# Performance work log

Measured on AMD Instinct MI355X. Metric: run time of the kernel, lower is better.

Reference implementation:

```python
import jax, jax.numpy as jnp
import numpy as np

N = 50000          # nodes
E = 500000         # edges (before self-loops)
IN_C = 128
OUT_C = 32
HEADS = 8
NEG_SLOPE = 0.2    # PyG GATConv default


def setup_inputs() -> dict:
    key = jax.random.key(0)
    k1, k2, k3, k4, k5 = jax.random.split(key, 5)
    x = jax.random.normal(k1, (N, IN_C), dtype=jnp.float32)
    edge_index = jax.random.randint(k2, (2, E), 0, N, dtype=jnp.int32)
    # learned params (PyG GATConv: shared lin, att_src/att_dst vectors, bias)
    s = 1.0 / np.sqrt(IN_C)
    W = jax.random.normal(k3, (IN_C, HEADS * OUT_C), dtype=jnp.float32) * s
    att_src = jax.random.normal(k4, (1, HEADS, OUT_C), dtype=jnp.float32) * s
    att_dst = jax.random.normal(k5, (1, HEADS, OUT_C), dtype=jnp.float32) * s
    bias = jnp.zeros((HEADS * OUT_C,), dtype=jnp.float32)
    return {"x": x, "edge_index": edge_index, "W": W,
            "att_src": att_src, "att_dst": att_dst, "bias": bias}


def reference(x, edge_index, W, att_src, att_dst, bias):
    n = x.shape[0]
    H, C = att_src.shape[1], att_src.shape[2]
    # Linear projection -> [N, H, C]
    xw = (x @ W).reshape(n, H, C)
    # Per-node attention logits [N, H]
    a_src = jnp.sum(xw * att_src, axis=-1)
    a_dst = jnp.sum(xw * att_dst, axis=-1)
    # add self-loops (PyG default add_self_loops=True)
    loop = jnp.arange(n, dtype=edge_index.dtype)
    src = jnp.concatenate([edge_index[0], loop])
    dst = jnp.concatenate([edge_index[1], loop])
    # edge scores: LeakyReLU(alpha_src[j] + alpha_dst[i])  -> [E+N, H]
    alpha = jax.nn.leaky_relu(a_src[src] + a_dst[dst], NEG_SLOPE)
    # segment softmax over edges grouped by destination node
    amax = jax.lax.stop_gradient(jax.ops.segment_max(alpha, dst, num_segments=n))
    alpha = jnp.exp(alpha - amax[dst])
    denom = jax.ops.segment_sum(alpha, dst, num_segments=n)
    alpha = alpha / (denom[dst] + 1e-16)
    # weighted messages and scatter-add aggregation
    msg = xw[src] * alpha[:, :, None]          # [E+N, H, C]
    out = jax.ops.segment_sum(msg, dst, num_segments=n)  # [N, H, C]
    return out.reshape(n, H * C) + bias
```

## Files before the change

### kernel.cpp

```cpp
#include <hip/hip_runtime.h>
#include <stdint.h>

#define N_NODES 50000
#define HC 256
#define IN_C 128
#define CAP 64
#define GEMM_BLKS 3125
#define EPB 160

typedef __bf16 v8bf __attribute__((ext_vector_type(8)));
typedef float  v4f  __attribute__((ext_vector_type(4)));

__device__ __forceinline__ uint16_t f2bf(float f) {
    union { float f; uint32_t i; } c; c.f = f;
    uint32_t x = c.i;
    uint32_t r = x + 0x7fffu + ((x >> 16) & 1u);
    return (uint16_t)(r >> 16);
}
__device__ __forceinline__ uint16_t f2h(float f) {
    union { _Float16 h; uint16_t u; } c;
    c.h = (_Float16)f;
    return c.u;
}
__device__ __forceinline__ void h8(uint4 u, float* f) {
    union { uint32_t i; _Float16 h[2]; } c;
    c.i = u.x; f[0] = (float)c.h[0]; f[1] = (float)c.h[1];
    c.i = u.y; f[2] = (float)c.h[0]; f[3] = (float)c.h[1];
    c.i = u.z; f[4] = (float)c.h[0]; f[5] = (float)c.h[1];
    c.i = u.w; f[6] = (float)c.h[0]; f[7] = (float)c.h[1];
}
__device__ __forceinline__ void ld4h(uint2 u, float& f0, float& f1, float& f2, float& f3) {
    union { uint32_t i; _Float16 h[2]; } c;
    c.i = u.x; f0 = (float)c.h[0]; f1 = (float)c.h[1];
    c.i = u.y; f2 = (float)c.h[0]; f3 = (float)c.h[1];
}
__device__ __forceinline__ float hexp2(float x) {
    return __builtin_amdgcn_exp2f(x);
}

__global__ void k_wt(const float* __restrict__ W, uint16_t* __restrict__ Wt,
                     int* __restrict__ cnt) {
    int idx = blockIdx.x * 256 + threadIdx.x;
    int k = idx >> 8;
    int c = idx & 255;
    Wt[c * IN_C + k] = f2bf(W[idx]);
    if (idx < 25000) *(int2*)(cnt + idx * 2) = make_int2(0, 0);
}

__global__ __launch_bounds__(256) void k_gemm_fill(const float* __restrict__ x,
                                                   const uint16_t* __restrict__ Wt,
                                                   const float* __restrict__ att_src,
                                                   const float* __restrict__ att_dst,
                                                   uint16_t* __restrict__ xwh,
                                                   float* __restrict__ a_src,
                                                   float* __restrict__ a_dst,
                                                   const int* __restrict__ src,
                                                   const int* __restrict__ dst,
                                                   int* __restrict__ cnt,
                                                   int* __restrict__ slots,
                                                   int E) {
    __shared__ uint16_t lsm[16 * 272];
    uint16_t* lx = lsm;
    uint16_t* lc = lsm;
    int t  = threadIdx.x;
    int nb = blockIdx.x * 16;

    int e = blockIdx.x * EPB + t;
    bool has = (t < EPB) && (e < E);
    int ed = 0, es = 0;
    if (has) { ed = dst[e]; es = src[e]; }

    {
        int row = t >> 4, c8 = (t & 15) * 8;
        const float4* p = (const float4*)(x + (size_t)(nb + row) * IN_C + c8);
        float4 p0 = p[0], p1 = p[1];
        v8bf a;
        a[0] = (__bf16)p0.x; a[1] = (__bf16)p0.y; a[2] = (__bf16)p0.z; a[3] = (__bf16)p0.w;
        a[4] = (__bf16)p1.x; a[5] = (__bf16)p1.y; a[6] = (__bf16)p1.z; a[7] = (__bf16)p1.w;
        *(v8bf*)(lx + row * 136 + c8) = a;
    }
    __syncthreads();

    int w = t >> 6, lane = t & 63;
    int m = lane & 15, g = lane >> 4;
    v4f acc[4];
#pragma unroll
    for (int ct = 0; ct < 4; ++ct) acc[ct] = (v4f){0.f, 0.f, 0.f, 0.f};
    const uint16_t* lxp = lx + m * 136 + g * 8;
    const uint16_t* wp  = Wt + (size_t)(w * 64 + m) * IN_C + g * 8;
#pragma unroll
    for (int s = 0; s < 4; ++s) {
        v8bf a = *(const v8bf*)(lxp + s * 32);
#pragma unroll
        for (int ct = 0; ct < 4; ++ct) {
            v8bf b = *(const v8bf*)(wp + (size_t)ct * 16 * IN_C + s * 32);
            acc[ct] = __builtin_amdgcn_mfma_f32_16x16x32_bf16(a, b, acc[ct], 0, 0, 0);
        }
    }
    __syncthreads();

#pragma unroll
    for (int ct = 0; ct < 4; ++ct) {
        int cols = w * 64 + ((ct ^ g) << 4) + m;
#pragma unroll
        for (int r = 0; r < 4; ++r) {
            lc[(g * 4 + r) * 272 + cols] = f2h(acc[ct][r]);
        }
    }
    __syncthreads();

    {
        int row = t >> 4;
        int c   = t & 15;
        int gg  = row >> 2;
        int sc0 = c ^ (gg << 1);
        int sc1 = sc0 + 16;
        const uint16_t* lr = lc + row * 272;
        uint4 u0 = *(const uint4*)(lr + sc0 * 8);
        uint4 u1 = *(const uint4*)(lr + sc1 * 8);
        size_t gb = (size_t)(nb + row) * HC + c * 8;
        *(uint4*)(xwh + gb)       = u0;
        *(uint4*)(xwh + gb + 128) = u1;

        float f0[8], f1[8];
        h8(u0, f0);
        h8(u1, f1);
        float4 as0 = *(const float4*)(att_src + c * 8);
        float4 as1 = *(const float4*)(att_src + c * 8 + 4);
        float4 as2 = *(const float4*)(att_src + 128 + c * 8);
        float4 as3 = *(const float4*)(att_src + 128 + c * 8 + 4);
        float4 ad0 = *(const float4*)(att_dst + c * 8);
        float4 ad1 = *(const float4*)(att_dst + c * 8 + 4);
        float4 ad2 = *(const float4*)(att_dst + 128 + c * 8);
        float4 ad3 = *(const float4*)(att_dst + 128 + c * 8 + 4);

        float ps0 = f0[0]*as0.x + f0[1]*as0.y + f0[2]*as0.z + f0[3]*as0.w
                  + f0[4]*as1.x + f0[5]*as1.y + f0[6]*as1.z + f0[7]*as1.w;
        float pd0 = f0[0]*ad0.x + f0[1]*ad0.y + f0[2]*ad0.z + f0[3]*ad0.w
                  + f0[4]*ad1.x + f0[5]*ad1.y + f0[6]*ad1.z + f0[7]*ad1.w;
        float ps1 = f1[0]*as2.x + f1[1]*as2.y + f1[2]*as2.z + f1[3]*as2.w
                  + f1[4]*as3.x + f1[5]*as3.y + f1[6]*as3.z + f1[7]*as3.w;
        float pd1 = f1[0]*ad2.x + f1[1]*ad2.y + f1[2]*ad2.z + f1[3]*ad2.w
                  + f1[4]*ad3.x + f1[5]*ad3.y + f1[6]*ad3.z + f1[7]*ad3.w;

        ps0 += __shfl_xor(ps0, 1, 64); ps0 += __shfl_xor(ps0, 2, 64);
        ps1 += __shfl_xor(ps1, 1, 64); ps1 += __shfl_xor(ps1, 2, 64);
        pd0 += __shfl_xor(pd0, 1, 64); pd0 += __shfl_xor(pd0, 2, 64);
        pd1 += __shfl_xor(pd1, 1, 64); pd1 += __shfl_xor(pd1, 2, 64);
        if ((c & 3) == 0) {
            const float LOG2E = 1.44269504f;
            int node = nb + row;
            int h = c >> 2;
            a_src[node * 8 + h]     = ps0 * LOG2E;
            a_src[node * 8 + 4 + h] = ps1 * LOG2E;
            a_dst[node * 8 + h]     = pd0 * LOG2E;
            a_dst[node * 8 + 4 + h] = pd1 * LOG2E;
        }
    }

    if (has) {
        int pos = atomicAdd(&cnt[ed], 1);
        slots[(size_t)ed * CAP + pos] = es;
    }
}

__global__ __launch_bounds__(256) void k_agg(const uint16_t* __restrict__ xwh,
                                             const float* __restrict__ a_src,
                                             const float* __restrict__ a_dst,
                                             const int* __restrict__ cnt,
                                             const int* __restrict__ slots,
                                             const float* __restrict__ bias,
                                             float* __restrict__ out) {
    int i    = blockIdx.x * 4 + (threadIdx.x >> 6);
    int lane = threadIdx.x & 63;
    int h = lane >> 3;
    float sdst = a_dst[i * 8 + h];

    float s0 = a_src[i * 8 + h] + sdst;
    s0 = fmaxf(s0, 0.2f * s0);
    float p0 = hexp2(s0);
    float l = p0;
    uint2 us = *(const uint2*)(xwh + (size_t)i * HC + lane * 4);
    float sx0, sx1, sx2, sx3;
    ld4h(us, sx0, sx1, sx2, sx3);
    float a0 = p0 * sx0, a1 = p0 * sx1, a2 = p0 * sx2, a3 = p0 * sx3;

    int n     = cnt[i];
    int start = i * CAP;
    int end   = start + n;
    int e = start;
    for (; e + 8 <= end; e += 8) {
        uint2 uu[8];
        float sa[8];
#pragma unroll
        for (int k = 0; k < 8; ++k) {
            int j = __builtin_amdgcn_readfirstlane(slots[e + k]);
            uu[k] = *(const uint2*)(xwh + (size_t)j * HC + lane * 4);
            sa[k] = a_src[j * 8 + h];
        }
#pragma unroll
        for (int k = 0; k < 8; ++k) {
            float s = sa[k] + sdst;
            s = fmaxf(s, 0.2f * s);
            float w = hexp2(s);
            l += w;
            float g0, g1, g2, g3;
            ld4h(uu[k], g0, g1, g2, g3);
            a0 = fmaf(w, g0, a0); a1 = fmaf(w, g1, a1);
            a2 = fmaf(w, g2, a2); a3 = fmaf(w, g3, a3);
        }
    }
    if (e < end) {
        uint2 uu[8];
        float sa[8];
#pragma unroll
        for (int k = 0; k < 8; ++k) {
            int jr = __builtin_amdgcn_readfirstlane(slots[e + k]);
            uint32_t j = min((uint32_t)jr, (uint32_t)(N_NODES - 1));
            uu[k] = *(const uint2*)(xwh + (size_t)j * HC + lane * 4);
            sa[k] = a_src[j * 8 + h];
        }
#pragma unroll
        for (int k = 0; k < 8; ++k) {
            float s = sa[k] + sdst;
            s = fmaxf(s, 0.2f * s);
            float w = (e + k < end) ? hexp2(s) : 0.f;
            l += w;
            float g0, g1, g2, g3;
            ld4h(uu[k], g0, g1, g2, g3);
            a0 = fmaf(w, g0, a0); a1 = fmaf(w, g1, a1);
            a2 = fmaf(w, g2, a2); a3 = fmaf(w, g3, a3);
        }
    }

    float inv = 1.f / (l + 1e-16f);
    float4 b = *(const float4*)(bias + lane * 4);
    float4 o;
    o.x = fmaf(a0, inv, b.x);
    o.y = fmaf(a1, inv, b.y);
    o.z = fmaf(a2, inv, b.z);
    o.w = fmaf(a3, inv, b.w);
    *(float4*)(out + (size_t)i * HC + lane * 4) = o;
}

extern "C" void kernel_launch(void* const* d_in, const int* in_sizes, int n_in,
                              void* d_out, int out_size, void* d_ws, size_t ws_size,
                              hipStream_t stream) {
    const float* x       = (const float*)d_in[0];
    const int*   ei      = (const int*)d_in[1];
    const float* W       = (const float*)d_in[2];
    const float* att_src = (const float*)d_in[3];
    const float* att_dst = (const float*)d_in[4];
    const float* bias    = (const float*)d_in[5];
    float*       out     = (float*)d_out;

    const int E = in_sizes[1] / 2;
    const int* src = ei;
    const int* dst = ei + E;

    char* ws = (char*)d_ws;
    uint16_t* xwh   = (uint16_t*)(ws);
    uint16_t* Wt    = (uint16_t*)(ws + 25600000);
    float*    a_src = (float*)   (ws + 25665536);
    float*    a_dst = (float*)   (ws + 27265536);
    int*      cnt   = (int*)     (ws + 28865536);
    int*      slots = (int*)     (ws + 29065536);

    k_wt<<<128, 256, 0, stream>>>(W, Wt, cnt);
    k_gemm_fill<<<GEMM_BLKS, 256, 0, stream>>>(x, Wt, att_src, att_dst,
                                               xwh, a_src, a_dst,
                                               src, dst, cnt, slots, E);
    k_agg<<<12500, 256, 0, stream>>>(xwh, a_src, a_dst, cnt, slots, bias, out);
}
```

Baseline: 174.5 us.

## Process 64 nodes per GEMM block to reuse W fragments across subtiles

Each GEMM block now handles 64 nodes instead of 16. W B-fragments are loaded once per k-step and reused across four 16-row subtiles, so blocks drop from 3125 to 782 and W traffic shrinks. Each block takes 640 edges (up to three per thread), and the edge-slot atomics now run right after staging x so they overlap the MFMA work. The cost is more registers (16 accumulators), launch_bounds(256,4), a serialized per-subtile epilogue with extra barriers, and bounds checks for the partial last block.

Result: no change. 174.7 us (+0.1%).

```diff
diff --git a/kernel.cpp b/kernel.cpp
--- a/kernel.cpp
+++ b/kernel.cpp
@@ -5,8 +5,9 @@
 #define HC 256
 #define IN_C 128
 #define CAP 64
-#define GEMM_BLKS 3125
-#define EPB 160
+#define NPB 64
+#define GEMM_BLKS 782
+#define EPB 640
 
 typedef __bf16 v8bf __attribute__((ext_vector_type(8)));
 typedef float  v4f  __attribute__((ext_vector_type(4)));
@@ -47,120 +48,148 @@
     if (idx < 25000) *(int2*)(cnt + idx * 2) = make_int2(0, 0);
 }
 
-__global__ __launch_bounds__(256) void k_gemm_fill(const float* __restrict__ x,
-                                                   const uint16_t* __restrict__ Wt,
-                                                   const float* __restrict__ att_src,
-                                                   const float* __restrict__ att_dst,
-                                                   uint16_t* __restrict__ xwh,
-                                                   float* __restrict__ a_src,
-                                                   float* __restrict__ a_dst,
-                                                   const int* __restrict__ src,
-                                                   const int* __restrict__ dst,
-                                                   int* __restrict__ cnt,
-                                                   int* __restrict__ slots,
-                                                   int E) {
-    __shared__ uint16_t lsm[16 * 272];
+__global__ __launch_bounds__(256, 4) void k_gemm_fill(const float* __restrict__ x,
+                                                      const uint16_t* __restrict__ Wt,
+                                                      const float* __restrict__ att_src,
+                                                      const float* __restrict__ att_dst,
+                                                      uint16_t* __restrict__ xwh,
+                                                      float* __restrict__ a_src,
+                                                      float* __restrict__ a_dst,
+                                                      const int* __restrict__ src,
+                                                      const int* __restrict__ dst,
+                                                      int* __restrict__ cnt,
+                                                      int* __restrict__ slots,
+                                                      int E) {
+    __shared__ uint16_t lsm[64 * 136];
     uint16_t* lx = lsm;
     uint16_t* lc = lsm;
     int t  = threadIdx.x;
-    int nb = blockIdx.x * 16;
-
-    int e = blockIdx.x * EPB + t;
-    bool has = (t < EPB) && (e < E);
-    int ed = 0, es = 0;
-    if (has) { ed = dst[e]; es = src[e]; }
+    int nb = blockIdx.x * NPB;
+
+    int e0 = blockIdx.x * EPB + t;
+    int e1 = e0 + 256;
+    int e2 = e0 + 512;
+    bool h0 = (e0 < E);
+    bool h1 = (e1 < E);
+    bool h2 = (t < 128) && (e2 < E);
+    int d0 = 0, s0 = 0, d1 = 0, s1 = 0, d2 = 0, s2 = 0;
+    if (h0) { d0 = dst[e0]; s0 = src[e0]; }
+    if (h1) { d1 = dst[e1]; s1 = src[e1]; }
+    if (h2) { d2 = dst[e2]; s2 = src[e2]; }
 
     {
-        int row = t >> 4, c8 = (t & 15) * 8;
-        const float4* p = (const float4*)(x + (size_t)(nb + row) * IN_C + c8);
-        float4 p0 = p[0], p1 = p[1];
-        v8bf a;
-        a[0] = (__bf16)p0.x; a[1] = (__bf16)p0.y; a[2] = (__bf16)p0.z; a[3] = (__bf16)p0.w;
-        a[4] = (__bf16)p1.x; a[5] = (__bf16)p1.y; a[6] = (__bf16)p1.z; a[7] = (__bf16)p1.w;
-        *(v8bf*)(lx + row * 136 + c8) = a;
+        int rr = t >> 4, c8 = (t & 15) * 8;
+#pragma unroll
+        for (int u = 0; u < 4; ++u) {
+            int row = rr + u * 16;
+            int nr  = nb + row;
+            v8bf a;
+#pragma unroll
+            for (int q = 0; q < 8; ++q) a[q] = (__bf16)0.f;
+            if (nr < N_NODES) {
+                const float4* p = (const float4*)(x + (size_t)nr * IN_C + c8);
+                float4 p0 = p[0], p1 = p[1];
+                a[0] = (__bf16)p0.x; a[1] = (__bf16)p0.y; a[2] = (__bf16)p0.z; a[3] = (__bf16)p0.w;
+                a[4] = (__bf16)p1.x; a[5] = (__bf16)p1.y; a[6] = (__bf16)p1.z; a[7] = (__bf16)p1.w;
+            }
+            *(v8bf*)(lx + row * 136 + c8) = a;
+        }
     }
     __syncthreads();
+
+    if (h0) { int pos = atomicAdd(&cnt[d0], 1); slots[(size_t)d0 * CAP + pos] = s0; }
+    if (h1) { int pos = atomicAdd(&cnt[d1], 1); slots[(size_t)d1 * CAP + pos] = s1; }
+    if (h2) { int pos = atomicAdd(&cnt[d2], 1); slots[(size_t)d2 * CAP + pos] = s2; }
 
     int w = t >> 6, lane = t & 63;
     int m = lane & 15, g = lane >> 4;
-    v4f acc[4];
-#pragma unroll
-    for (int ct = 0; ct < 4; ++ct) acc[ct] = (v4f){0.f, 0.f, 0.f, 0.f};
-    const uint16_t* lxp = lx + m * 136 + g * 8;
-    const uint16_t* wp  = Wt + (size_t)(w * 64 + m) * IN_C + g * 8;
+    v4f acc[4][4];
+#pragma unroll
+    for (int st = 0; st < 4; ++st)
+#pragma unroll
+        for (int ct = 0; ct < 4; ++ct) acc[st][ct] = (v4f){0.f, 0.f, 0.f, 0.f};
+
+    const uint16_t* wp = Wt + (size_t)(w * 64 + m) * IN_C + g * 8;
 #pragma unroll
     for (int s = 0; s < 4; ++s) {
-        v8bf a = *(const v8bf*)(lxp + s * 32);
+        v8bf b0 = *(const v8bf*)(wp + (size_t)0 * 16 * IN_C + s * 32);
+        v8bf b1 = *(const v8bf*)(wp + (size_t)1 * 16 * IN_C + s * 32);
+        v8bf b2 = *(const v8bf*)(wp + (size_t)2 * 16 * IN_C + s * 32);
+        v8bf b3 = *(const v8bf*)(wp + (size_t)3 * 16 * IN_C + s * 32);
+#pragma unroll
+        for (int st = 0; st < 4; ++st) {
+            v8bf a = *(const v8bf*)(lx + (st * 16 + m) * 136 + g * 8 + s * 32);
+            acc[st][0] = __builtin_amdgcn_mfma_f32_16x16x32_bf16(a, b0, acc[st][0], 0, 0, 0);
+            acc[st][1] = __builtin_amdgcn_mfma_f32_16x16x32_bf16(a, b1, acc[st][1], 0, 0, 0);
+            acc[st][2] = __builtin_amdgcn_mfma_f32_16x16x32_bf16(a, b2, acc[st][2], 0, 0, 0);
+            acc[st][3] = __builtin_amdgcn_mfma_f32_16x16x32_bf16(a, b3, acc[st][3], 0, 0, 0);
+        }
+    }
+    __syncthreads();
+
+#pragma unroll
+    for (int st = 0; st < 4; ++st) {
 #pragma unroll
         for (int ct = 0; ct < 4; ++ct) {
-            v8bf b = *(const v8bf*)(wp + (size_t)ct * 16 * IN_C + s * 32);
-            acc[ct] = __builtin_amdgcn_mfma_f32_16x16x32_bf16(a, b, acc[ct], 0, 0, 0);
-        }
-    }
-    __syncthreads();
-
-#pragma unroll
-    for (int ct = 0; ct < 4; ++ct) {
-        int cols = w * 64 + ((ct ^ g) << 4) + m;
-#pragma unroll
-        for (int r = 0; r < 4; ++r) {
-            lc[(g * 4 + r) * 272 + cols] = f2h(acc[ct][r]);
-        }
-    }
-    __syncthreads();
-
-    {
-        int row = t >> 4;
-        int c   = t & 15;
-        int gg  = row >> 2;
-        int sc0 = c ^ (gg << 1);
-        int sc1 = sc0 + 16;
-        const uint16_t* lr = lc + row * 272;
-        uint4 u0 = *(const uint4*)(lr + sc0 * 8);
-        uint4 u1 = *(const uint4*)(lr + sc1 * 8);
-        size_t gb = (size_t)(nb + row) * HC + c * 8;
-        *(uint4*)(xwh + gb)       = u0;
-        *(uint4*)(xwh + gb + 128) = u1;
-
-        float f0[8], f1[8];
-        h8(u0, f0);
-        h8(u1, f1);
-        float4 as0 = *(const float4*)(att_src + c * 8);
-        float4 as1 = *(const float4*)(att_src + c * 8 + 4);
-        float4 as2 = *(const float4*)(att_src + 128 + c * 8);
-        float4 as3 = *(const float4*)(att_src + 128 + c * 8 + 4);
-        float4 ad0 = *(const float4*)(att_dst + c * 8);
-        float4 ad1 = *(const float4*)(att_dst + c * 8 + 4);
-        float4 ad2 = *(const float4*)(att_dst + 128 + c * 8);
-        float4 ad3 = *(const float4*)(att_dst + 128 + c * 8 + 4);
-
-        float ps0 = f0[0]*as0.x + f0[1]*as0.y + f0[2]*as0.z + f0[3]*as0.w
-                  + f0[4]*as1.x + f0[5]*as1.y + f0[6]*as1.z + f0[7]*as1.w;
-        float pd0 = f0[0]*ad0.x + f0[1]*ad0.y + f0[2]*ad0.z + f0[3]*ad0.w
-                  + f0[4]*ad1.x + f0[5]*ad1.y + f0[6]*ad1.z + f0[7]*ad1.w;
-        float ps1 = f1[0]*as2.x + f1[1]*as2.y + f1[2]*as2.z + f1[3]*as2.w
-                  + f1[4]*as3.x + f1[5]*as3.y + f1[6]*as3.z + f1[7]*as3.w;
-        float pd1 = f1[0]*ad2.x + f1[1]*ad2.y + f1[2]*ad2.z + f1[3]*ad2.w
-                  + f1[4]*ad3.x + f1[5]*ad3.y + f1[6]*ad3.z + f1[7]*ad3.w;
-
-        ps0 += __shfl_xor(ps0, 1, 64); ps0 += __shfl_xor(ps0, 2, 64);
-        ps1 += __shfl_xor(ps1, 1, 64); ps1 += __shfl_xor(ps1, 2, 64);
-        pd0 += __shfl_xor(pd0, 1, 64); pd0 += __shfl_xor(pd0, 2, 64);
-        pd1 += __shfl_xor(pd1, 1, 64); pd1 += __shfl_xor(pd1, 2, 64);
-        if ((c & 3) == 0) {
-            const float LOG2E = 1.44269504f;
-            int node = nb + row;
-            int h = c >> 2;
-            a_src[node * 8 + h]     = ps0 * LOG2E;
-            a_src[node * 8 + 4 + h] = ps1 * LOG2E;
-            a_dst[node * 8 + h]     = pd0 * LOG2E;
-            a_dst[node * 8 + 4 + h] = pd1 * LOG2E;
-        }
-    }
-
-    if (has) {
-        int pos = atomicAdd(&cnt[ed], 1);
-        slots[(size_t)ed * CAP + pos] = es;
+            int cols = w * 64 + ((ct ^ g) << 4) + m;
+#pragma unroll
+            for (int r = 0; r < 4; ++r) {
+                lc[(g * 4 + r) * 272 + cols] = f2h(acc[st][ct][r]);
+            }
+        }
+        __syncthreads();
+
+        {
+            int row = t >> 4;
+            int c   = t & 15;
+            int gg  = row >> 2;
+            int sc0 = c ^ (gg << 1);
+            int sc1 = sc0 + 16;
+            const uint16_t* lr = lc + row * 272;
+            uint4 u0 = *(const uint4*)(lr + sc0 * 8);
+            uint4 u1 = *(const uint4*)(lr + sc1 * 8);
+            int node = nb + st * 16 + row;
+            if (node < N_NODES) {
+                size_t gb = (size_t)node * HC + c * 8;
+                *(uint4*)(xwh + gb)       = u0;
+                *(uint4*)(xwh + gb + 128) = u1;
+            }
+
+            float f0[8], f1[8];
+            h8(u0, f0);
+            h8(u1, f1);
+            float4 as0 = *(const float4*)(att_src + c * 8);
+            float4 as1 = *(const float4*)(att_src + c * 8 + 4);
+            float4 as2 = *(const float4*)(att_src + 128 + c * 8);
+            float4 as3 = *(const float4*)(att_src + 128 + c * 8 + 4);
+            float4 ad0 = *(const float4*)(att_dst + c * 8);
+            float4 ad1 = *(const float4*)(att_dst + c * 8 + 4);
+            float4 ad2 = *(const float4*)(att_dst + 128 + c * 8);
+            float4 ad3 = *(const float4*)(att_dst + 128 + c * 8 + 4);
+
+            float ps0 = f0[0]*as0.x + f0[1]*as0.y + f0[2]*as0.z + f0[3]*as0.w
+                      + f0[4]*as1.x + f0[5]*as1.y + f0[6]*as1.z + f0[7]*as1.w;
+            float pd0 = f0[0]*ad0.x + f0[1]*ad0.y + f0[2]*ad0.z + f0[3]*ad0.w
+                      + f0[4]*ad1.x + f0[5]*ad1.y + f0[6]*ad1.z + f0[7]*ad1.w;
+            float ps1 = f1[0]*as2.x + f1[1]*as2.y + f1[2]*as2.z + f1[3]*as2.w
+                      + f1[4]*as3.x + f1[5]*as3.y + f1[6]*as3.z + f1[7]*as3.w;
+            float pd1 = f1[0]*ad2.x + f1[1]*ad2.y + f1[2]*ad2.z + f1[3]*ad2.w
+                      + f1[4]*ad3.x + f1[5]*ad3.y + f1[6]*ad3.z + f1[7]*ad3.w;
+
+            ps0 += __shfl_xor(ps0, 1, 64); ps0 += __shfl_xor(ps0, 2, 64);
+            ps1 += __shfl_xor(ps1, 1, 64); ps1 += __shfl_xor(ps1, 2, 64);
+            pd0 += __shfl_xor(pd0, 1, 64); pd0 += __shfl_xor(pd0, 2, 64);
+            pd1 += __shfl_xor(pd1, 1, 64); pd1 += __shfl_xor(pd1, 2, 64);
+            if ((c & 3) == 0 && node < N_NODES) {
+                const float LOG2E = 1.44269504f;
+                int h = c >> 2;
+                a_src[node * 8 + h]     = ps0 * LOG2E;
+                a_src[node * 8 + 4 + h] = ps1 * LOG2E;
+                a_dst[node * 8 + h]     = pd0 * LOG2E;
+                a_dst[node * 8 + 4 + h] = pd1 * LOG2E;
+            }
+        }
+        __syncthreads();
     }
 }
 
```
